# Performance work log

Hardware: AMD Instinct MI355X
Metric: run time of the kernel (lower is better)

The kernel has to match this reference:

```python
import jax, jax.numpy as jnp
import numpy as np

N_SRC, N_DST, N_EDGES = 50000, 50000, 500000
IN_DIM, OUT_DIM, EDGE_DIM = 128, 128, 11
BN_EPS = 1e-5


def setup_inputs() -> dict:
    key = jax.random.key(0)
    ks = jax.random.split(key, 16)
    s = 0.05
    return {
        "src_feat": jax.random.normal(ks[0], (N_SRC, IN_DIM), jnp.float32),
        "dst_feat": jax.random.normal(ks[1], (N_DST, IN_DIM), jnp.float32),
        "edge_feats": jax.random.normal(ks[2], (N_EDGES, EDGE_DIM), jnp.float32),
        "src_idx": jax.random.randint(ks[3], (N_EDGES,), 0, N_SRC, jnp.int32),
        "dst_idx": jax.random.randint(ks[4], (N_EDGES,), 0, N_DST, jnp.int32),
        "W_src": jax.random.normal(ks[5], (IN_DIM, OUT_DIM), jnp.float32) * s,
        "b_src": jnp.zeros((OUT_DIM,), jnp.float32),
        "W_dst": jax.random.normal(ks[6], (IN_DIM, OUT_DIM), jnp.float32) * s,
        "b_dst": jnp.zeros((OUT_DIM,), jnp.float32),
        "W_edge": jax.random.normal(ks[7], (EDGE_DIM, OUT_DIM), jnp.float32) * s,
        "b_edge": jnp.zeros((OUT_DIM,), jnp.float32),
        "attn_w": jax.random.normal(ks[8], (3 * OUT_DIM,), jnp.float32) * s,
        "attn_b": jnp.zeros((), jnp.float32),
        "gamma": jnp.ones((OUT_DIM,), jnp.float32),
        "beta": jnp.zeros((OUT_DIM,), jnp.float32),
        "alpha": jnp.asarray(0.25, jnp.float32),
    }


def reference(src_feat, dst_feat, edge_feats, src_idx, dst_idx,
              W_src, b_src, W_dst, b_dst, W_edge, b_edge,
              attn_w, attn_b, gamma, beta, alpha):
    D = W_src.shape[1]
    # project at node/edge level (math identical to projecting gathered feats)
    hs = src_feat @ W_src + b_src            # [Ns, D]  (linear_src)
    hd = dst_feat @ W_dst + b_dst            # [Nd, D]  (linear_dst)
    ep = edge_feats @ W_edge + b_edge        # [E, D]   (linear_edge)
    # attn_l on concat([src, dst, edge]) == sum of three dot products + bias
    aw_s, aw_d, aw_e = attn_w[:D], attn_w[D:2 * D], attn_w[2 * D:]
    a = (hs @ aw_s)[src_idx] + (hd @ aw_d)[dst_idx] + ep @ aw_e + attn_b  # [E]
    # edge softmax over incoming edges of each dst node
    n_dst = dst_feat.shape[0]
    seg_max = jax.ops.segment_max(a, dst_idx, num_segments=n_dst)
    a_exp = jnp.exp(a - seg_max[dst_idx])
    denom = jax.ops.segment_sum(a_exp, dst_idx, num_segments=n_dst)
    attn = a_exp / denom[dst_idx]            # [E]
    # weighted message = attn * linear_src(src_h); scatter-sum to dst
    msg = attn[:, None] * hs[src_idx]        # [E, D]
    h_new = jax.ops.segment_sum(msg, dst_idx, num_segments=n_dst)  # [Nd, D]
    # BatchNorm1d (training-mode batch statistics)
    mean = jnp.mean(h_new, axis=0)
    var = jnp.var(h_new, axis=0)
    h_bn = (h_new - mean) / jnp.sqrt(var + BN_EPS) * gamma + beta
    # PReLU (single shared alpha); dropout is identity in eval
    return jnp.where(h_bn >= 0, h_bn, alpha * h_bn)
```

## Files before the change

kernel.cpp:

```cpp
#include <hip/hip_runtime.h>
#include <cstddef>

#define NSRC 50000
#define NDST 50000
#define NEDGE 500000
#define DIM 128
#define EDIM 11
#define BN_EPS 1e-5f
#define SCAN_NBLK ((NDST + 255) / 256)

#define HS_BLOCKS ((NSRC + 63) / 64)
#define DS_BLOCKS ((NDST + 31) / 32)
#define ED_BLOCKS ((NEDGE + 511) / 512)
#define SC_BLOCKS ((NEDGE + 1023) / 1024)

typedef short bf16x8 __attribute__((ext_vector_type(8)));
typedef float f32x4 __attribute__((ext_vector_type(4)));

#define OFF_HS       0
#define OFF_SSCORE   (OFF_HS + (size_t)NSRC*DIM/2)
#define OFF_DSCORE   (OFF_SSCORE + NSRC)
#define OFF_EE       (OFF_DSCORE + NDST)
#define OFF_DEG16    (OFF_EE + NEDGE)
#define OFF_COLSUM   (OFF_DEG16 + (size_t)NDST*16)
#define OFF_COLSQ    (OFF_COLSUM + 128)
#define OFF_OFFS     (OFF_COLSQ + 128)
#define OFF_RANK     (OFF_OFFS + NDST + 2)
#define OFF_PAIRS    (OFF_RANK + NEDGE)
#define OFF_WDVEC    (OFF_PAIRS + 2*(size_t)NEDGE)
#define OFF_WEVEC    (OFF_WDVEC + 128)
#define OFF_SCAL     (OFF_WEVEC + 16)
#define OFF_PART     (OFF_SCAL + 4)
#define OFF_WT       (((OFF_PART + 256 + 3) / 4) * 4)

__device__ __forceinline__ unsigned short f2bf(float x) {
    unsigned int u = __float_as_uint(x);
    u += 0x7FFFu + ((u >> 16) & 1u);
    return (unsigned short)(u >> 16);
}
__device__ __forceinline__ float bf2f(unsigned int u16) {
    return __uint_as_float(u16 << 16);
}

__global__ void k_prep(const float* __restrict__ W_dst, const float* __restrict__ b_dst,
                       const float* __restrict__ W_edge, const float* __restrict__ b_edge,
                       const float* __restrict__ attn_w, const float* __restrict__ attn_b,
                       float* __restrict__ wd_vec, float* __restrict__ we_vec,
                       float* __restrict__ scal) {
    int t = threadIdx.x;
    float acc = 0.f;
    for (int d = 0; d < DIM; ++d) acc += W_dst[t * DIM + d] * attn_w[DIM + d];
    wd_vec[t] = acc;
    if (t < EDIM) {
        float e = 0.f;
        for (int d = 0; d < DIM; ++d) e += W_edge[t * DIM + d] * attn_w[2 * DIM + d];
        we_vec[t] = e;
    }
    __shared__ float red[128];
    red[t] = b_dst[t] * attn_w[DIM + t];
    __syncthreads();
    for (int s = 64; s > 0; s >>= 1) { if (t < s) red[t] += red[t + s]; __syncthreads(); }
    if (t == 0) scal[0] = red[0];
    __syncthreads();
    red[t] = b_edge[t] * attn_w[2 * DIM + t];
    __syncthreads();
    for (int s = 64; s > 0; s >>= 1) { if (t < s) red[t] += red[t + s]; __syncthreads(); }
    if (t == 0) scal[1] = red[0] + attn_b[0];
}

__global__ __launch_bounds__(256) void k_wt(const float* __restrict__ W,
                                            unsigned short* __restrict__ wt) {
    __shared__ float tile[32][33];
    int bi = blockIdx.x & 3;
    int bj = blockIdx.x >> 2;
    int t = threadIdx.x;
    int cl = t & 31;
    #pragma unroll
    for (int i = 0; i < 4; ++i) {
        int kl = (t >> 5) * 4 + i;
        tile[kl][cl] = W[(size_t)(bi * 32 + kl) * DIM + bj * 32 + cl];
    }
    __syncthreads();
    int ko = t & 31;
    #pragma unroll
    for (int i = 0; i < 4; ++i) {
        int co = (t >> 5) * 4 + i;
        wt[(size_t)(bj * 32 + co) * DIM + bi * 32 + ko] = f2bf(tile[ko][co]);
    }
}

__global__ __launch_bounds__(256, 2) void k_fused(const float* __restrict__ A,
                                               const unsigned short* __restrict__ wt,
                                               const float* __restrict__ bias,
                                               const float* __restrict__ attn_w,
                                               const float* __restrict__ B,
                                               const float* __restrict__ ef,
                                               const int* __restrict__ dst_idx,
                                               const float* __restrict__ wd_vec,
                                               const float* __restrict__ we_vec,
                                               const float* __restrict__ scal,
                                               unsigned short* __restrict__ hsb,
                                               float* __restrict__ s_score,
                                               float* __restrict__ d_score,
                                               float* __restrict__ ee,
                                               int* __restrict__ deg16,
                                               int* __restrict__ rank) {
    const int bid = blockIdx.x;
    const int t = threadIdx.x;

    if (bid < HS_BLOCKS) {
        const int wv = t >> 6;
        const int lane = t & 63;
        const int lrow = lane & 15;
        const int kg = lane >> 4;
        const int grow = bid * 64 + wv * 16 + lrow;
        const bool rowok = grow < NSRC;
        const float* arow = A + (size_t)grow * DIM;

        bf16x8 af[4];
        #pragma unroll
        for (int s = 0; s < 4; ++s) {
            float4 p0 = make_float4(0.f, 0.f, 0.f, 0.f), p1 = p0;
            if (rowok) {
                p0 = *reinterpret_cast<const float4*>(arow + 32 * s + kg * 8);
                p1 = *reinterpret_cast<const float4*>(arow + 32 * s + kg * 8 + 4);
            }
            bf16x8 a;
            a[0] = (short)f2bf(p0.x); a[1] = (short)f2bf(p0.y);
            a[2] = (short)f2bf(p0.z); a[3] = (short)f2bf(p0.w);
            a[4] = (short)f2bf(p1.x); a[5] = (short)f2bf(p1.y);
            a[6] = (short)f2bf(p1.z); a[7] = (short)f2bf(p1.w);
            af[s] = a;
        }

        f32x4 acc[8];
        #pragma unroll
        for (int c = 0; c < 8; ++c) acc[c] = (f32x4){0.f, 0.f, 0.f, 0.f};

        #pragma unroll
        for (int c = 0; c < 8; ++c) {
            #pragma unroll
            for (int s = 0; s < 4; ++s) {
                const bf16x8 b = *reinterpret_cast<const bf16x8*>(
                    wt + ((size_t)(16 * c + lrow) * DIM + 32 * s + kg * 8));
                acc[c] = __builtin_amdgcn_mfma_f32_16x16x32_bf16(af[s], b, acc[c], 0, 0, 0);
            }
        }

        float p[4] = {0.f, 0.f, 0.f, 0.f};
        #pragma unroll
        for (int c = 0; c < 8; ++c) {
            float bb = bias[16 * c + lrow];
            float aw = attn_w[16 * c + lrow];
            #pragma unroll
            for (int i = 0; i < 4; ++i) {
                float v = acc[c][i] + bb;
                acc[c][i] = v;
                p[i] += v * aw;
            }
        }
        #pragma unroll
        for (int i = 0; i < 4; ++i) {
            p[i] += __shfl_xor(p[i], 1);
            p[i] += __shfl_xor(p[i], 2);
            p[i] += __shfl_xor(p[i], 4);
            p[i] += __shfl_xor(p[i], 8);
        }
        const int orow0 = bid * 64 + wv * 16 + kg * 4;
        #pragma unroll
        for (int c = 0; c < 8; ++c) {
            #pragma unroll
            for (int i = 0; i < 4; ++i) {
                unsigned int mybf = f2bf(acc[c][i]);
                unsigned int nb = (unsigned int)__shfl_xor((int)mybf, 1);
                int orow = orow0 + i;
                if ((lrow & 1) == 0 && orow < NSRC) {
                    *reinterpret_cast<unsigned int*>(hsb + (size_t)orow * DIM + 16 * c + lrow)
                        = (mybf & 0xFFFFu) | (nb << 16);
                }
            }
        }
        #pragma unroll
        for (int i = 0; i < 4; ++i) {
            int orow = orow0 + i;
            if (lrow == 0 && orow < NSRC) s_score[orow] = p[i];
        }
    } else if (bid < HS_BLOCKS + DS_BLOCKS) {
        int row = (bid - HS_BLOCKS) * 32 + (t >> 3);
        int c0 = (t & 7) * 16;
        if (row >= NDST) return;
        const float4* x = reinterpret_cast<const float4*>(B + (size_t)row * DIM + c0);
        const float4* w = reinterpret_cast<const float4*>(wd_vec + c0);
        float p = 0.f;
        #pragma unroll
        for (int i = 0; i < 4; ++i) {
            float4 a = x[i], b = w[i];
            p += a.x * b.x + a.y * b.y + a.z * b.z + a.w * b.w;
        }
        p += __shfl_xor(p, 1);
        p += __shfl_xor(p, 2);
        p += __shfl_xor(p, 4);
        if ((t & 7) == 0) d_score[row] = p + scal[0];
    } else {
        float wvv[EDIM];
        #pragma unroll
        for (int k = 0; k < EDIM; ++k) wvv[k] = we_vec[k];
        const float s1 = scal[1];
        int ebase = (bid - HS_BLOCKS - DS_BLOCKS) * 512 + t;
        #pragma unroll
        for (int i = 0; i < 2; ++i) {
            int e = ebase + i * 256;
            if (e < NEDGE) {
                const float* er = ef + (size_t)e * EDIM;
                float a = s1;
                #pragma unroll
                for (int k = 0; k < EDIM; ++k) a += er[k] * wvv[k];
                ee[e] = a;
                int d = dst_idx[e];
                rank[e] = atomicAdd(&deg16[(size_t)d * 16], 1);
            }
        }
    }
}

__global__ __launch_bounds__(256) void k_scanA(const int* __restrict__ deg16,
                                               int* __restrict__ off,
                                               int* __restrict__ partials) {
    __shared__ int tmp[256];
    int t = threadIdx.x;
    int i = blockIdx.x * 256 + t;
    int v = (i < NDST) ? deg16[(size_t)i * 16] : 0;
    tmp[t] = v;
    __syncthreads();
    #pragma unroll
    for (int d = 1; d < 256; d <<= 1) {
        int u = (t >= d) ? tmp[t - d] : 0;
        __syncthreads();
        tmp[t] += u;
        __syncthreads();
    }
    if (i < NDST) off[i] = tmp[t] - v;
    if (t == 255) partials[blockIdx.x] = tmp[255];
}

__global__ __launch_bounds__(256) void k_scanB(int* __restrict__ partials) {
    __shared__ int tmp[256];
    int t = threadIdx.x;
    int v = (t < SCAN_NBLK) ? partials[t] : 0;
    tmp[t] = v;
    __syncthreads();
    #pragma unroll
    for (int d = 1; d < 256; d <<= 1) {
        int u = (t >= d) ? tmp[t - d] : 0;
        __syncthreads();
        tmp[t] += u;
        __syncthreads();
    }
    if (t < SCAN_NBLK) partials[t] = tmp[t] - v;
}

__global__ __launch_bounds__(256) void k_scanC(int* __restrict__ off,
                                               const int* __restrict__ partials) {
    int t = threadIdx.x;
    int i = blockIdx.x * 256 + t;
    if (i < NDST) off[i] += partials[blockIdx.x];
    if (i == 0) off[NDST] = NEDGE;
}

__global__ __launch_bounds__(256) void k_scat(const int* __restrict__ src_idx,
                                              const int* __restrict__ dst_idx,
                                              const float* __restrict__ ee,
                                              const float* __restrict__ s_score,
                                              const float* __restrict__ d_score,
                                              const int* __restrict__ off,
                                              const int* __restrict__ rank,
                                              int2* __restrict__ pairs) {
    int base = blockIdx.x * 1024 + threadIdx.x;
    #pragma unroll
    for (int i = 0; i < 4; ++i) {
        int e = base + i * 256;
        if (e < NEDGE) {
            int s = src_idx[e], d = dst_idx[e];
            float w = expf(ee[e] + s_score[s] + d_score[d]);
            int pos = off[d] + rank[e];
            pairs[pos] = make_int2(s, __float_as_int(w));
        }
    }
}

__global__ __launch_bounds__(256) void k_gather(const unsigned short* __restrict__ hsb,
                                                const int* __restrict__ off,
                                                const int2* __restrict__ pairs,
                                                float* __restrict__ h_new) {
    int wid = (blockIdx.x * blockDim.x + threadIdx.x) >> 6;
    int lane = threadIdx.x & 63;
    if (wid >= NDST) return;
    int b = off[wid], e2 = off[wid + 1];
    int deg = e2 - b;
    float ax = 0.f, ay = 0.f, wsum = 0.f;

    for (int base = 0; base < deg; base += 64) {
        int cnt = min(deg - base, 64);
        int myS = 0;
        float myW = 0.f;
        if (lane < cnt) {
            int2 p = pairs[b + base + lane];
            myS = p.x;
            myW = __int_as_float(p.y);
        }
        wsum += myW;

        int j = 0;
        for (; j + 4 <= cnt; j += 4) {
            int s0 = __shfl(myS, j + 0), s1 = __shfl(myS, j + 1);
            int s2 = __shfl(myS, j + 2), s3 = __shfl(myS, j + 3);
            float w0 = __shfl(myW, j + 0), w1 = __shfl(myW, j + 1);
            float w2 = __shfl(myW, j + 2), w3 = __shfl(myW, j + 3);
            unsigned int v0 = *reinterpret_cast<const unsigned int*>(hsb + (size_t)s0 * DIM + 2 * lane);
            unsigned int v1 = *reinterpret_cast<const unsigned int*>(hsb + (size_t)s1 * DIM + 2 * lane);
            unsigned int v2 = *reinterpret_cast<const unsigned int*>(hsb + (size_t)s2 * DIM + 2 * lane);
            unsigned int v3 = *reinterpret_cast<const unsigned int*>(hsb + (size_t)s3 * DIM + 2 * lane);
            ax += w0 * bf2f(v0 & 0xFFFFu) + w1 * bf2f(v1 & 0xFFFFu)
                + w2 * bf2f(v2 & 0xFFFFu) + w3 * bf2f(v3 & 0xFFFFu);
            ay += w0 * bf2f(v0 >> 16) + w1 * bf2f(v1 >> 16)
                + w2 * bf2f(v2 >> 16) + w3 * bf2f(v3 >> 16);
        }
        for (; j < cnt; ++j) {
            int s0 = __shfl(myS, j);
            float w0 = __shfl(myW, j);
            unsigned int v0 = *reinterpret_cast<const unsigned int*>(hsb + (size_t)s0 * DIM + 2 * lane);
            ax += w0 * bf2f(v0 & 0xFFFFu);
            ay += w0 * bf2f(v0 >> 16);
        }
    }

    #pragma unroll
    for (int m = 1; m < 64; m <<= 1) wsum += __shfl_xor(wsum, m);

    float inv = (deg > 0) ? 1.f / wsum : 0.f;
    reinterpret_cast<float2*>(h_new + (size_t)wid * DIM)[lane] = make_float2(ax * inv, ay * inv);
}

__global__ __launch_bounds__(256) void k_bnstats(const float* __restrict__ h,
                                                 float* __restrict__ colsum,
                                                 float* __restrict__ colsq) {
    int col = threadIdx.x & 127;
    int rp = threadIdx.x >> 7;
    float s = 0.f, q = 0.f;
    for (int r = blockIdx.x * 2 + rp; r < NDST; r += gridDim.x * 2) {
        float x = h[(size_t)r * DIM + col];
        s += x;
        q += x * x;
    }
    __shared__ float ls[2][128], lq[2][128];
    ls[rp][col] = s;
    lq[rp][col] = q;
    __syncthreads();
    if (rp == 0) {
        atomicAdd(&colsum[col], ls[0][col] + ls[1][col]);
        atomicAdd(&colsq[col], lq[0][col] + lq[1][col]);
    }
}

__global__ __launch_bounds__(256) void k_bnfinal(float* __restrict__ h,
                                                 const float* __restrict__ colsum,
                                                 const float* __restrict__ colsq,
                                                 const float* __restrict__ gamma,
                                                 const float* __restrict__ beta,
                                                 const float* __restrict__ alpha_p) {
    const size_t total4 = (size_t)NDST * DIM / 4;
    const float alpha = alpha_p[0];
    const float invN = 1.f / (float)NDST;
    const int c0 = (threadIdx.x & 31) * 4;
    float sc[4], sh[4];
    #pragma unroll
    for (int k = 0; k < 4; ++k) {
        float mean = colsum[c0 + k] * invN;
        float var = colsq[c0 + k] * invN - mean * mean;
        float s = gamma[c0 + k] * rsqrtf(var + BN_EPS);
        sc[k] = s;
        sh[k] = beta[c0 + k] - mean * s;
    }
    size_t stride = (size_t)gridDim.x * blockDim.x;
    for (size_t i = blockIdx.x * blockDim.x + threadIdx.x; i < total4; i += stride) {
        float4 x = reinterpret_cast<float4*>(h)[i];
        float y0 = x.x * sc[0] + sh[0];
        float y1 = x.y * sc[1] + sh[1];
        float y2 = x.z * sc[2] + sh[2];
        float y3 = x.w * sc[3] + sh[3];
        float4 o;
        o.x = y0 >= 0.f ? y0 : alpha * y0;
        o.y = y1 >= 0.f ? y1 : alpha * y1;
        o.z = y2 >= 0.f ? y2 : alpha * y2;
        o.w = y3 >= 0.f ? y3 : alpha * y3;
        reinterpret_cast<float4*>(h)[i] = o;
    }
}

extern "C" void kernel_launch(void* const* d_in, const int* in_sizes, int n_in,
                              void* d_out, int out_size, void* d_ws, size_t ws_size,
                              hipStream_t stream) {
    const float* src_feat   = (const float*)d_in[0];
    const float* dst_feat   = (const float*)d_in[1];
    const float* edge_feats = (const float*)d_in[2];
    const int*   src_idx    = (const int*)d_in[3];
    const int*   dst_idx    = (const int*)d_in[4];
    const float* W_src      = (const float*)d_in[5];
    const float* b_src      = (const float*)d_in[6];
    const float* W_dst      = (const float*)d_in[7];
    const float* b_dst      = (const float*)d_in[8];
    const float* W_edge     = (const float*)d_in[9];
    const float* b_edge     = (const float*)d_in[10];
    const float* attn_w     = (const float*)d_in[11];
    const float* attn_b     = (const float*)d_in[12];
    const float* gamma      = (const float*)d_in[13];
    const float* beta       = (const float*)d_in[14];
    const float* alpha      = (const float*)d_in[15];

    float* ws      = (float*)d_ws;
    unsigned short* hsb = (unsigned short*)(ws + OFF_HS);
    float* s_score = ws + OFF_SSCORE;
    float* d_score = ws + OFF_DSCORE;
    float* ee      = ws + OFF_EE;
    int*   deg16   = (int*)(ws + OFF_DEG16);
    float* colsum  = ws + OFF_COLSUM;
    float* colsq   = ws + OFF_COLSQ;
    int*   off     = (int*)(ws + OFF_OFFS);
    int*   rank    = (int*)(ws + OFF_RANK);
    int2*  pairs   = (int2*)(ws + OFF_PAIRS);
    float* wd_vec  = ws + OFF_WDVEC;
    float* we_vec  = ws + OFF_WEVEC;
    float* scal    = ws + OFF_SCAL;
    int*   part    = (int*)(ws + OFF_PART);
    unsigned short* wt = (unsigned short*)(ws + OFF_WT);

    float* h_new = (float*)d_out;

    hipMemsetAsync(deg16, 0, ((size_t)NDST * 16 + 256) * sizeof(int), stream);

    k_prep<<<1, 128, 0, stream>>>(W_dst, b_dst, W_edge, b_edge, attn_w, attn_b,
                                  wd_vec, we_vec, scal);
    k_wt<<<16, 256, 0, stream>>>(W_src, wt);
    k_fused<<<HS_BLOCKS + DS_BLOCKS + ED_BLOCKS, 256, 0, stream>>>(
        src_feat, wt, b_src, attn_w, dst_feat, edge_feats, dst_idx,
        wd_vec, we_vec, scal, hsb, s_score, d_score, ee, deg16, rank);
    k_scanA<<<SCAN_NBLK, 256, 0, stream>>>(deg16, off, part);
    k_scanB<<<1, 256, 0, stream>>>(part);
    k_scanC<<<SCAN_NBLK, 256, 0, stream>>>(off, part);
    k_scat<<<SC_BLOCKS, 256, 0, stream>>>(src_idx, dst_idx, ee, s_score, d_score,
                                          off, rank, pairs);
    k_gather<<<(NDST * 64 + 255) / 256, 256, 0, stream>>>(hsb, off, pairs, h_new);
    k_bnstats<<<512, 256, 0, stream>>>(h_new, colsum, colsq);
    k_bnfinal<<<1024, 256, 0, stream>>>(h_new, colsum, colsq, gamma, beta, alpha);
}
```

Baseline: 142.8 us.

## Precompute node scores separately, compute edge exp in fused kernel, widen gather loads

Source scores are now computed with a folded W_src·attn vector in a separate score kernel alongside dst scores, instead of inside the MFMA projection. The fused kernel interleaves projection and edge blocks and evaluates the full edge logit and exp there, so the scatter kernel only permutes precomputed weights. The gather kernel splits each wave into two halves processing different edges with 8-byte loads, reducing shuffles per element. This adds an extra launch and reads src_feat twice. Scores now come from fp32 rather than bf16-projected values, and the exp is still taken without subtracting a segment max.

Result: faster. 139.5 us (-2.3%).

```diff
diff --git a/kernel.cpp b/kernel.cpp
--- a/kernel.cpp
+++ b/kernel.cpp
@@ -11,8 +11,9 @@
 
 #define HS_BLOCKS ((NSRC + 63) / 64)
 #define DS_BLOCKS ((NDST + 31) / 32)
-#define ED_BLOCKS ((NEDGE + 511) / 512)
+#define EDB       ((NEDGE + 511) / 512)
 #define SC_BLOCKS ((NEDGE + 1023) / 1024)
+#define FUSE_GRID (196 * 9)
 
 typedef short bf16x8 __attribute__((ext_vector_type(8)));
 typedef float f32x4 __attribute__((ext_vector_type(4)));
@@ -20,8 +21,8 @@
 #define OFF_HS       0
 #define OFF_SSCORE   (OFF_HS + (size_t)NSRC*DIM/2)
 #define OFF_DSCORE   (OFF_SSCORE + NSRC)
-#define OFF_EE       (OFF_DSCORE + NDST)
-#define OFF_DEG16    (OFF_EE + NEDGE)
+#define OFF_EW       (OFF_DSCORE + NDST)
+#define OFF_DEG16    (OFF_EW + NEDGE)
 #define OFF_COLSUM   (OFF_DEG16 + (size_t)NDST*16)
 #define OFF_COLSQ    (OFF_COLSUM + 128)
 #define OFF_OFFS     (OFF_COLSQ + 128)
@@ -30,7 +31,8 @@
 #define OFF_WDVEC    (OFF_PAIRS + 2*(size_t)NEDGE)
 #define OFF_WEVEC    (OFF_WDVEC + 128)
 #define OFF_SCAL     (OFF_WEVEC + 16)
-#define OFF_PART     (OFF_SCAL + 4)
+#define OFF_WSVEC    (OFF_SCAL + 4)
+#define OFF_PART     (OFF_WSVEC + 128)
 #define OFF_WT       (((OFF_PART + 256 + 3) / 4) * 4)
 
 __device__ __forceinline__ unsigned short f2bf(float x) {
@@ -44,28 +46,40 @@
 
 __global__ void k_prep(const float* __restrict__ W_dst, const float* __restrict__ b_dst,
                        const float* __restrict__ W_edge, const float* __restrict__ b_edge,
+                       const float* __restrict__ W_src, const float* __restrict__ b_src,
                        const float* __restrict__ attn_w, const float* __restrict__ attn_b,
                        float* __restrict__ wd_vec, float* __restrict__ we_vec,
-                       float* __restrict__ scal) {
-    int t = threadIdx.x;
-    float acc = 0.f;
-    for (int d = 0; d < DIM; ++d) acc += W_dst[t * DIM + d] * attn_w[DIM + d];
-    wd_vec[t] = acc;
-    if (t < EDIM) {
-        float e = 0.f;
-        for (int d = 0; d < DIM; ++d) e += W_edge[t * DIM + d] * attn_w[2 * DIM + d];
-        we_vec[t] = e;
-    }
+                       float* __restrict__ ws_vec, float* __restrict__ scal) {
+    int t = threadIdx.x;
+    int bb = blockIdx.x;
     __shared__ float red[128];
-    red[t] = b_dst[t] * attn_w[DIM + t];
-    __syncthreads();
-    for (int s = 64; s > 0; s >>= 1) { if (t < s) red[t] += red[t + s]; __syncthreads(); }
-    if (t == 0) scal[0] = red[0];
-    __syncthreads();
-    red[t] = b_edge[t] * attn_w[2 * DIM + t];
-    __syncthreads();
-    for (int s = 64; s > 0; s >>= 1) { if (t < s) red[t] += red[t + s]; __syncthreads(); }
-    if (t == 0) scal[1] = red[0] + attn_b[0];
+    if (bb == 0) {
+        float acc = 0.f;
+        for (int d = 0; d < DIM; ++d) acc += W_dst[t * DIM + d] * attn_w[DIM + d];
+        wd_vec[t] = acc;
+        red[t] = b_dst[t] * attn_w[DIM + t];
+        __syncthreads();
+        for (int s = 64; s > 0; s >>= 1) { if (t < s) red[t] += red[t + s]; __syncthreads(); }
+        if (t == 0) scal[0] = red[0];
+    } else if (bb == 1) {
+        if (t < EDIM) {
+            float e = 0.f;
+            for (int d = 0; d < DIM; ++d) e += W_edge[t * DIM + d] * attn_w[2 * DIM + d];
+            we_vec[t] = e;
+        }
+        red[t] = b_edge[t] * attn_w[2 * DIM + t];
+        __syncthreads();
+        for (int s = 64; s > 0; s >>= 1) { if (t < s) red[t] += red[t + s]; __syncthreads(); }
+        if (t == 0) scal[1] = red[0] + attn_b[0];
+    } else {
+        float acc = 0.f;
+        for (int d = 0; d < DIM; ++d) acc += W_src[t * DIM + d] * attn_w[d];
+        ws_vec[t] = acc;
+        red[t] = b_src[t] * attn_w[t];
+        __syncthreads();
+        for (int s = 64; s > 0; s >>= 1) { if (t < s) red[t] += red[t + s]; __syncthreads(); }
+        if (t == 0) scal[2] = red[0];
+    }
 }
 
 __global__ __launch_bounds__(256) void k_wt(const float* __restrict__ W,
@@ -89,31 +103,68 @@
     }
 }
 
+__global__ __launch_bounds__(256) void k_score(const float* __restrict__ src_feat,
+                                               const float* __restrict__ dst_feat,
+                                               const float* __restrict__ ws_vec,
+                                               const float* __restrict__ wd_vec,
+                                               const float* __restrict__ scal,
+                                               float* __restrict__ s_score,
+                                               float* __restrict__ d_score) {
+    int bid = blockIdx.x;
+    const float* X;
+    const float* V;
+    float* out;
+    float c;
+    int r0;
+    if (bid < DS_BLOCKS) {
+        X = src_feat; V = ws_vec; out = s_score; c = scal[2]; r0 = bid * 32;
+    } else {
+        X = dst_feat; V = wd_vec; out = d_score; c = scal[0]; r0 = (bid - DS_BLOCKS) * 32;
+    }
+    int t = threadIdx.x;
+    int row = r0 + (t >> 3);
+    int c0 = (t & 7) * 16;
+    if (row >= NDST) return;
+    const float4* x = reinterpret_cast<const float4*>(X + (size_t)row * DIM + c0);
+    const float4* w = reinterpret_cast<const float4*>(V + c0);
+    float p = 0.f;
+    #pragma unroll
+    for (int i = 0; i < 4; ++i) {
+        float4 a = x[i], b = w[i];
+        p += a.x * b.x + a.y * b.y + a.z * b.z + a.w * b.w;
+    }
+    p += __shfl_xor(p, 1);
+    p += __shfl_xor(p, 2);
+    p += __shfl_xor(p, 4);
+    if ((t & 7) == 0) out[row] = p + c;
+}
+
 __global__ __launch_bounds__(256, 2) void k_fused(const float* __restrict__ A,
                                                const unsigned short* __restrict__ wt,
                                                const float* __restrict__ bias,
-                                               const float* __restrict__ attn_w,
-                                               const float* __restrict__ B,
                                                const float* __restrict__ ef,
+                                               const int* __restrict__ src_idx,
                                                const int* __restrict__ dst_idx,
-                                               const float* __restrict__ wd_vec,
+                                               const float* __restrict__ s_score,
+                                               const float* __restrict__ d_score,
                                                const float* __restrict__ we_vec,
                                                const float* __restrict__ scal,
                                                unsigned short* __restrict__ hsb,
-                                               float* __restrict__ s_score,
-                                               float* __restrict__ d_score,
-                                               float* __restrict__ ee,
+                                               float* __restrict__ ew,
                                                int* __restrict__ deg16,
                                                int* __restrict__ rank) {
-    const int bid = blockIdx.x;
+    const int g = blockIdx.x / 9;
+    const int sl = blockIdx.x % 9;
     const int t = threadIdx.x;
 
-    if (bid < HS_BLOCKS) {
+    if (sl < 4) {
+        const int hb = g * 4 + sl;
+        if (hb >= HS_BLOCKS) return;
         const int wv = t >> 6;
         const int lane = t & 63;
         const int lrow = lane & 15;
         const int kg = lane >> 4;
-        const int grow = bid * 64 + wv * 16 + lrow;
+        const int grow = hb * 64 + wv * 16 + lrow;
         const bool rowok = grow < NSRC;
         const float* arow = A + (size_t)grow * DIM;
 
@@ -147,31 +198,13 @@
             }
         }
 
-        float p[4] = {0.f, 0.f, 0.f, 0.f};
+        const int orow0 = hb * 64 + wv * 16 + kg * 4;
         #pragma unroll
         for (int c = 0; c < 8; ++c) {
             float bb = bias[16 * c + lrow];
-            float aw = attn_w[16 * c + lrow];
             #pragma unroll
             for (int i = 0; i < 4; ++i) {
-                float v = acc[c][i] + bb;
-                acc[c][i] = v;
-                p[i] += v * aw;
-            }
-        }
-        #pragma unroll
-        for (int i = 0; i < 4; ++i) {
-            p[i] += __shfl_xor(p[i], 1);
-            p[i] += __shfl_xor(p[i], 2);
-            p[i] += __shfl_xor(p[i], 4);
-            p[i] += __shfl_xor(p[i], 8);
-        }
-        const int orow0 = bid * 64 + wv * 16 + kg * 4;
-        #pragma unroll
-        for (int c = 0; c < 8; ++c) {
-            #pragma unroll
-            for (int i = 0; i < 4; ++i) {
-                unsigned int mybf = f2bf(acc[c][i]);
+                unsigned int mybf = f2bf(acc[c][i] + bb);
                 unsigned int nb = (unsigned int)__shfl_xor((int)mybf, 1);
                 int orow = orow0 + i;
                 if ((lrow & 1) == 0 && orow < NSRC) {
@@ -180,43 +213,25 @@
                 }
             }
         }
-        #pragma unroll
-        for (int i = 0; i < 4; ++i) {
-            int orow = orow0 + i;
-            if (lrow == 0 && orow < NSRC) s_score[orow] = p[i];
-        }
-    } else if (bid < HS_BLOCKS + DS_BLOCKS) {
-        int row = (bid - HS_BLOCKS) * 32 + (t >> 3);
-        int c0 = (t & 7) * 16;
-        if (row >= NDST) return;
-        const float4* x = reinterpret_cast<const float4*>(B + (size_t)row * DIM + c0);
-        const float4* w = reinterpret_cast<const float4*>(wd_vec + c0);
-        float p = 0.f;
-        #pragma unroll
-        for (int i = 0; i < 4; ++i) {
-            float4 a = x[i], b = w[i];
-            p += a.x * b.x + a.y * b.y + a.z * b.z + a.w * b.w;
-        }
-        p += __shfl_xor(p, 1);
-        p += __shfl_xor(p, 2);
-        p += __shfl_xor(p, 4);
-        if ((t & 7) == 0) d_score[row] = p + scal[0];
     } else {
+        const int eb = g * 5 + (sl - 4);
+        if (eb >= EDB) return;
         float wvv[EDIM];
         #pragma unroll
         for (int k = 0; k < EDIM; ++k) wvv[k] = we_vec[k];
         const float s1 = scal[1];
-        int ebase = (bid - HS_BLOCKS - DS_BLOCKS) * 512 + t;
+        int ebase = eb * 512 + t;
         #pragma unroll
         for (int i = 0; i < 2; ++i) {
             int e = ebase + i * 256;
             if (e < NEDGE) {
+                int s = src_idx[e], d = dst_idx[e];
                 const float* er = ef + (size_t)e * EDIM;
                 float a = s1;
                 #pragma unroll
                 for (int k = 0; k < EDIM; ++k) a += er[k] * wvv[k];
-                ee[e] = a;
-                int d = dst_idx[e];
+                a += s_score[s] + d_score[d];
+                ew[e] = expf(a);
                 rank[e] = atomicAdd(&deg16[(size_t)d * 16], 1);
             }
         }
@@ -269,9 +284,7 @@
 
 __global__ __launch_bounds__(256) void k_scat(const int* __restrict__ src_idx,
                                               const int* __restrict__ dst_idx,
-                                              const float* __restrict__ ee,
-                                              const float* __restrict__ s_score,
-                                              const float* __restrict__ d_score,
+                                              const float* __restrict__ ew,
                                               const int* __restrict__ off,
                                               const int* __restrict__ rank,
                                               int2* __restrict__ pairs) {
@@ -280,10 +293,9 @@
     for (int i = 0; i < 4; ++i) {
         int e = base + i * 256;
         if (e < NEDGE) {
-            int s = src_idx[e], d = dst_idx[e];
-            float w = expf(ee[e] + s_score[s] + d_score[d]);
+            int d = dst_idx[e];
             int pos = off[d] + rank[e];
-            pairs[pos] = make_int2(s, __float_as_int(w));
+            pairs[pos] = make_int2(src_idx[e], __float_as_int(ew[e]));
         }
     }
 }
@@ -297,7 +309,9 @@
     if (wid >= NDST) return;
     int b = off[wid], e2 = off[wid + 1];
     int deg = e2 - b;
-    float ax = 0.f, ay = 0.f, wsum = 0.f;
+    const int half = lane >> 5;
+    const int c8 = lane & 31;
+    float a0 = 0.f, a1 = 0.f, a2 = 0.f, a3 = 0.f, wsum = 0.f;
 
     for (int base = 0; base < deg; base += 64) {
         int cnt = min(deg - base, 64);
@@ -311,34 +325,43 @@
         wsum += myW;
 
         int j = 0;
-        for (; j + 4 <= cnt; j += 4) {
-            int s0 = __shfl(myS, j + 0), s1 = __shfl(myS, j + 1);
-            int s2 = __shfl(myS, j + 2), s3 = __shfl(myS, j + 3);
-            float w0 = __shfl(myW, j + 0), w1 = __shfl(myW, j + 1);
-            float w2 = __shfl(myW, j + 2), w3 = __shfl(myW, j + 3);
-            unsigned int v0 = *reinterpret_cast<const unsigned int*>(hsb + (size_t)s0 * DIM + 2 * lane);
-            unsigned int v1 = *reinterpret_cast<const unsigned int*>(hsb + (size_t)s1 * DIM + 2 * lane);
-            unsigned int v2 = *reinterpret_cast<const unsigned int*>(hsb + (size_t)s2 * DIM + 2 * lane);
-            unsigned int v3 = *reinterpret_cast<const unsigned int*>(hsb + (size_t)s3 * DIM + 2 * lane);
-            ax += w0 * bf2f(v0 & 0xFFFFu) + w1 * bf2f(v1 & 0xFFFFu)
-                + w2 * bf2f(v2 & 0xFFFFu) + w3 * bf2f(v3 & 0xFFFFu);
-            ay += w0 * bf2f(v0 >> 16) + w1 * bf2f(v1 >> 16)
-                + w2 * bf2f(v2 >> 16) + w3 * bf2f(v3 >> 16);
-        }
-        for (; j < cnt; ++j) {
-            int s0 = __shfl(myS, j);
-            float w0 = __shfl(myW, j);
-            unsigned int v0 = *reinterpret_cast<const unsigned int*>(hsb + (size_t)s0 * DIM + 2 * lane);
-            ax += w0 * bf2f(v0 & 0xFFFFu);
-            ay += w0 * bf2f(v0 >> 16);
-        }
-    }
-
+        for (; j + 8 <= cnt; j += 8) {
+            #pragma unroll
+            for (int q = 0; q < 4; ++q) {
+                int jj = j + 2 * q + half;
+                int s0 = __shfl(myS, jj);
+                float w0 = __shfl(myW, jj);
+                uint2 v = *reinterpret_cast<const uint2*>(hsb + (size_t)s0 * DIM + c8 * 4);
+                a0 += w0 * bf2f(v.x & 0xFFFFu);
+                a1 += w0 * bf2f(v.x >> 16);
+                a2 += w0 * bf2f(v.y & 0xFFFFu);
+                a3 += w0 * bf2f(v.y >> 16);
+            }
+        }
+        for (; j < cnt; j += 2) {
+            int jj = j + half;
+            int s0 = __shfl(myS, jj);
+            float w0 = __shfl(myW, jj);
+            uint2 v = *reinterpret_cast<const uint2*>(hsb + (size_t)s0 * DIM + c8 * 4);
+            a0 += w0 * bf2f(v.x & 0xFFFFu);
+            a1 += w0 * bf2f(v.x >> 16);
+            a2 += w0 * bf2f(v.y & 0xFFFFu);
+            a3 += w0 * bf2f(v.y >> 16);
+        }
+    }
+
+    a0 += __shfl_xor(a0, 32);
+    a1 += __shfl_xor(a1, 32);
+    a2 += __shfl_xor(a2, 32);
+    a3 += __shfl_xor(a3, 32);
     #pragma unroll
     for (int m = 1; m < 64; m <<= 1) wsum += __shfl_xor(wsum, m);
 
     float inv = (deg > 0) ? 1.f / wsum : 0.f;
-    reinterpret_cast<float2*>(h_new + (size_t)wid * DIM)[lane] = make_float2(ax * inv, ay * inv);
+    if (half == 0) {
+        reinterpret_cast<float4*>(h_new + (size_t)wid * DIM)[c8]
+            = make_float4(a0 * inv, a1 * inv, a2 * inv, a3 * inv);
+    }
 }
 
 __global__ __launch_bounds__(256) void k_bnstats(const float* __restrict__ h,
@@ -421,7 +444,7 @@
     unsigned short* hsb = (unsigned short*)(ws + OFF_HS);
     float* s_score = ws + OFF_SSCORE;
     float* d_score = ws + OFF_DSCORE;
-    float* ee      = ws + OFF_EE;
+    float* ew      = ws + OFF_EW;
     int*   deg16   = (int*)(ws + OFF_DEG16);
     float* colsum  = ws + OFF_COLSUM;
     float* colsq   = ws + OFF_COLSQ;
@@ -431,6 +454,7 @@
     float* wd_vec  = ws + OFF_WDVEC;
     float* we_vec  = ws + OFF_WEVEC;
     float* scal    = ws + OFF_SCAL;
+    float* ws_vec  = ws + OFF_WSVEC;
     int*   part    = (int*)(ws + OFF_PART);
     unsigned short* wt = (unsigned short*)(ws + OFF_WT);
 
@@ -438,17 +462,18 @@
 
     hipMemsetAsync(deg16, 0, ((size_t)NDST * 16 + 256) * sizeof(int), stream);
 
-    k_prep<<<1, 128, 0, stream>>>(W_dst, b_dst, W_edge, b_edge, attn_w, attn_b,
-                                  wd_vec, we_vec, scal);
+    k_prep<<<3, 128, 0, stream>>>(W_dst, b_dst, W_edge, b_edge, W_src, b_src,
+                                  attn_w, attn_b, wd_vec, we_vec, ws_vec, scal);
     k_wt<<<16, 256, 0, stream>>>(W_src, wt);
-    k_fused<<<HS_BLOCKS + DS_BLOCKS + ED_BLOCKS, 256, 0, stream>>>(
-        src_feat, wt, b_src, attn_w, dst_feat, edge_feats, dst_idx,
-        wd_vec, we_vec, scal, hsb, s_score, d_score, ee, deg16, rank);
+    k_score<<<2 * DS_BLOCKS, 256, 0, stream>>>(src_feat, dst_feat, ws_vec, wd_vec,
+                                               scal, s_score, d_score);
+    k_fused<<<FUSE_GRID, 256, 0, stream>>>(src_feat, wt, b_src, edge_feats,
+                                           src_idx, dst_idx, s_score, d_score,
+                                           we_vec, scal, hsb, ew, deg16, rank);
     k_scanA<<<SCAN_NBLK, 256, 0, stream>>>(deg16, off, part);
     k_scanB<<<1, 256, 0, stream>>>(part);
     k_scanC<<<SCAN_NBLK, 256, 0, stream>>>(off, part);
-    k_scat<<<SC_BLOCKS, 256, 0, stream>>>(src_idx, dst_idx, ee, s_score, d_score,
-                                          off, rank, pairs);
+    k_scat<<<SC_BLOCKS, 256, 0, stream>>>(src_idx, dst_idx, ew, off, rank, pairs);
     k_gather<<<(NDST * 64 + 255) / 256, 256, 0, stream>>>(hsb, off, pairs, h_new);
     k_bnstats<<<512, 256, 0, stream>>>(h_new, colsum, colsq);
     k_bnfinal<<<1024, 256, 0, stream>>>(h_new, colsum, colsq, gamma, beta, alpha);
```
